# Optimization experiments

Hardware: AMD Instinct MI355X
Metric: run time of the kernel (lower is better)

The kernel has to match this reference:

```python
import jax, jax.numpy as jnp
import numpy as np

B, T, D, V = 64, 512, 1024, 28


def setup_inputs() -> dict:
    key = jax.random.key(0)
    ks = jax.random.split(key, 8)
    s = 0.05  # 'random_normal' keras initializer stddev
    return {
        "x": jax.random.normal(ks[0], (B, T, D), jnp.float32),
        "Wa": jax.random.normal(ks[1], (V, 1), jnp.float32) * s,
        "Ua": jax.random.normal(ks[2], (D, 1), jnp.float32) * s,
        "Va": jax.random.normal(ks[3], (1, 1), jnp.float32) * s,
        "Wo": jax.random.normal(ks[4], (V, 1), jnp.float32) * s,
        "Uo": jax.random.normal(ks[5], (D, V), jnp.float32) * s,
        "Co": jax.random.normal(ks[6], (D, V), jnp.float32) * s,
        "emb_table": jax.random.normal(ks[7], (V, V), jnp.float32) * s,
    }


def reference(x, Wa, Ua, Va, Wo, Uo, Co, emb_table):
    # x: [B, T, D]
    Bs, Ts, Ds = x.shape
    UaH = x @ Ua                                   # [B,T,1], step-invariant
    # Hanterior at step t is x[:, t-1] (zeros at t=0): it is updated AFTER y_t
    h_prev_seq = jnp.concatenate(
        [jnp.zeros((Bs, 1, Ds), x.dtype), x[:, :-1]], axis=1)  # [B,T,D]

    def step(y_prev, h_prev):
        # y_prev: [B,V]   h_prev: [B,D]
        WaS = y_prev @ Wa                          # [B,1]
        scores = jnp.tanh(UaH + WaS[:, None, :]) @ Va   # [B,T,1]
        # original applies softmax over the last (size-1) axis -> all ones; kept faithful
        scores = jax.nn.softmax(scores, axis=-1)
        c = jnp.einsum('btd,bt->bd', x, scores[..., 0])  # [B,D] context
        # keras Embedding casts its (float) input to int indices
        idx = y_prev.astype(jnp.int32)             # [B,V], values in [0, V)
        emb_res = emb_table[idx]                   # [B,V,V]
        WoE = (emb_res @ Wo)[..., 0]               # [B,V]
        y = jax.nn.sigmoid(WoE + h_prev @ Uo + c @ Co)   # [B,V]
        return y, y

    y0 = jnp.zeros((Bs, V), x.dtype)
    _, ys = jax.lax.scan(step, y0, jnp.swapaxes(h_prev_seq, 0, 1))  # [T,B,V]
    return jnp.swapaxes(ys, 0, 1)                  # [B,T,V]
```

## Files before the change

### kernel.cpp

```cpp
#include <hip/hip_runtime.h>
#include <cstddef>

#define BB 64
#define TT 512
#define DD 1024
#define VV 28
#define BV (BB * VV)

__global__ __launch_bounds__(256, 4) void k1_hU_rowsum(
    const float* __restrict__ x, const float* __restrict__ Uo,
    float* __restrict__ hU, float* __restrict__ part) {
  __shared__ float xs[32][68];
  __shared__ float Wl[64][32];
  const int g   = blockIdx.x;
  const int b   = g >> 4;
  const int tch = g & 15;
  const int t0  = tch << 5;
  const int tid = threadIdx.x;
  const int row = tid & 31;
  const int vg  = tid >> 5;
  const int vbase = vg << 2;
  float acc[4] = {0.f, 0.f, 0.f, 0.f};
  const float* xbase = x + (size_t)(b * TT + t0) * DD;

  for (int c = 0; c < 16; ++c) {
    const int d0 = c << 6;
    __syncthreads();
#pragma unroll
    for (int i = 0; i < 2; ++i) {
      const int f = tid + (i << 8);
      const int r = f >> 4;
      const int col = (f & 15) << 2;
      *reinterpret_cast<float4*>(&xs[r][col]) =
          *reinterpret_cast<const float4*>(xbase + (size_t)r * DD + d0 + col);
    }
#pragma unroll
    for (int k = 0; k < 8; ++k) {
      const int idx = tid + (k << 8);
      const int r = idx >> 5, ccol = idx & 31;
      Wl[r][ccol] = (ccol < VV) ? Uo[(size_t)(d0 + r) * VV + ccol] : 0.f;
    }
    __syncthreads();
#pragma unroll 2
    for (int dd = 0; dd < 64; dd += 4) {
      const float4 xv = *reinterpret_cast<const float4*>(&xs[row][dd]);
      const float xq[4] = {xv.x, xv.y, xv.z, xv.w};
#pragma unroll
      for (int q = 0; q < 4; ++q) {
        const float4 wa = *reinterpret_cast<const float4*>(&Wl[dd + q][vbase]);
        acc[0] = fmaf(xq[q], wa.x, acc[0]);
        acc[1] = fmaf(xq[q], wa.y, acc[1]);
        acc[2] = fmaf(xq[q], wa.z, acc[2]);
        acc[3] = fmaf(xq[q], wa.w, acc[3]);
      }
    }
    if (tid < 64) {
      float s = 0.f;
#pragma unroll 8
      for (int r = 0; r < 32; ++r) s += xs[r][tid];
      part[(size_t)(b * 16 + tch) * DD + d0 + tid] = s;
    }
  }
  const int t = t0 + row;
  if (t + 1 < TT && vbase < VV) {
    float* o = hU + (size_t)(t + 1) * BV + b * VV + vbase;
    *reinterpret_cast<float4*>(o) = make_float4(acc[0], acc[1], acc[2], acc[3]);
  }
}

__global__ __launch_bounds__(256) void k2_ctx_ew(
    const float* __restrict__ part, const float* __restrict__ Co,
    const float* __restrict__ Wo, const float* __restrict__ emb,
    float* __restrict__ ctx, float* __restrict__ ew) {
  __shared__ float rs[DD];
  __shared__ float red[8][32];
  const int b = blockIdx.x;
  const int tid = threadIdx.x;
  for (int d = tid; d < DD; d += 256) {
    float s = 0.f;
#pragma unroll
    for (int k = 0; k < 16; ++k) s += part[(size_t)(b * 16 + k) * DD + d];
    rs[d] = s;
  }
  __syncthreads();
  const int v = tid & 31, seg = tid >> 5;
  float pa = 0.f;
  if (v < VV) {
    const float* cp = Co + (size_t)(seg * 128) * VV + v;
    const float* rp = &rs[seg * 128];
#pragma unroll 4
    for (int d = 0; d < 128; ++d) pa = fmaf(rp[d], cp[(size_t)d * VV], pa);
  }
  red[seg][v] = pa;
  __syncthreads();
  if (tid < 32) {
    float s = 0.f;
#pragma unroll
    for (int k = 0; k < 8; ++k) s += red[k][tid];
    if (tid < VV) ctx[b * VV + tid] = s;
  }
  if (b == 0 && tid >= 64 && tid < 64 + VV) {
    const int j = tid - 64;
    float s = 0.f;
#pragma unroll
    for (int k = 0; k < VV; ++k) s = fmaf(emb[j * VV + k], Wo[k], s);
    ew[j] = s;
  }
}

__global__ __launch_bounds__(256) void k3a_bits(
    const float* __restrict__ hU, const float* __restrict__ ctx,
    const float* __restrict__ ew,
    unsigned long long* __restrict__ W0, unsigned long long* __restrict__ W1) {
  const int flat = blockIdx.x * 256 + threadIdx.x;
  const int t = flat / BV;
  const int bv = flat - t * BV;
  const float ctxv = ctx[bv];
  const float e0 = ew[0] + ctxv;
  const float e1 = ew[1] + ctxv;
  const float h = (t == 0) ? 0.f : hU[(size_t)t * BV + bv];
  const float c0 = 1.f / (1.f + expf(-(e0 + h)));
  const float c1 = 1.f / (1.f + expf(-(e1 + h)));
  const unsigned long long m0 = __ballot(c0 == 1.0f);
  const unsigned long long m1 = __ballot(c1 == 1.0f);
  if ((threadIdx.x & 63) == 0) {
    const int w = bv >> 6;
    W0[t * 28 + w] = m0;
    W1[t * 28 + w] = m1;
  }
}

__global__ __launch_bounds__(64) void k3b_scan(
    const unsigned long long* __restrict__ W0,
    const unsigned long long* __restrict__ W1,
    unsigned long long* __restrict__ S) {
  __shared__ unsigned long long l0[TT], l1[TT], ls[TT];
  const int j = blockIdx.x;
  const int tid = threadIdx.x;
  for (int t = tid; t < TT; t += 64) {
    l0[t] = W0[t * 28 + j];
    l1[t] = W1[t * 28 + j];
  }
  __syncthreads();
  if (tid == 0) {
    unsigned long long s = 0ull;
#pragma unroll 8
    for (int t = 0; t < TT; ++t) {
      ls[t] = s;
      s = (s & l1[t]) | (~s & l0[t]);
    }
  }
  __syncthreads();
  for (int t = tid; t < TT; t += 64) S[t * 28 + j] = ls[t];
}

__global__ __launch_bounds__(256) void k3c_out(
    const float* __restrict__ hU, const float* __restrict__ ctx,
    const float* __restrict__ ew, const unsigned long long* __restrict__ S,
    float* __restrict__ out) {
  const int flat = blockIdx.x * 256 + threadIdx.x;
  const int t = flat / BV;
  const int bv = flat - t * BV;
  const int b = bv / VV;
  const int v = bv - b * VV;
  const float ctxv = ctx[bv];
  const float h = (t == 0) ? 0.f : hU[(size_t)t * BV + bv];
  const unsigned long long w = S[t * 28 + (bv >> 6)];
  const float e = ((w >> (bv & 63)) & 1ull) ? ew[1] : ew[0];
  const float y = 1.f / (1.f + expf(-((e + ctxv) + h)));
  out[(size_t)b * TT * VV + (size_t)t * VV + v] = y;
}

extern "C" void kernel_launch(void* const* d_in, const int* in_sizes, int n_in,
                              void* d_out, int out_size, void* d_ws, size_t ws_size,
                              hipStream_t stream) {
  const float* x   = (const float*)d_in[0];
  const float* Wo  = (const float*)d_in[4];
  const float* Uo  = (const float*)d_in[5];
  const float* Co  = (const float*)d_in[6];
  const float* emb = (const float*)d_in[7];
  float* out = (float*)d_out;

  float* ws   = (float*)d_ws;
  float* hU   = ws;
  float* part = hU + (size_t)TT * BV;
  float* ctx  = part + (size_t)BB * 16 * DD;
  float* ewp  = ctx + BV;
  unsigned long long* W0 = (unsigned long long*)(ewp + 32);
  unsigned long long* W1 = W0 + (size_t)TT * 28;
  unsigned long long* S  = W1 + (size_t)TT * 28;

  k1_hU_rowsum<<<1024, 256, 0, stream>>>(x, Uo, hU, part);
  k2_ctx_ew<<<BB, 256, 0, stream>>>(part, Co, Wo, emb, ctx, ewp);
  k3a_bits<<<3584, 256, 0, stream>>>(hU, ctx, ewp, W0, W1);
  k3b_scan<<<28, 64, 0, stream>>>(W0, W1, S);
  k3c_out<<<3584, 256, 0, stream>>>(hU, ctx, ewp, S, out);
}
```

Baseline: 307.5 us.

## Restructure x@Uo kernel: one row per thread, all 28 outputs, split-D partials

```diff
diff --git a/kernel.cpp b/kernel.cpp
--- a/kernel.cpp
+++ b/kernel.cpp
@@ -7,64 +7,72 @@
 #define VV 28
 #define BV (BB * VV)
 
-__global__ __launch_bounds__(256, 4) void k1_hU_rowsum(
+template <int NDS>
+__global__ __launch_bounds__(256, 2) void k1_hU_rowsum(
     const float* __restrict__ x, const float* __restrict__ Uo,
-    float* __restrict__ hU, float* __restrict__ part) {
-  __shared__ float xs[32][68];
-  __shared__ float Wl[64][32];
+    float* __restrict__ hUp, float* __restrict__ part) {
+  constexpr int DPB = DD / NDS;
+  constexpr int NCH = DPB / 64;
+  __shared__ float xs[256][68];
   const int g   = blockIdx.x;
-  const int b   = g >> 4;
-  const int tch = g & 15;
-  const int t0  = tch << 5;
+  const int ds  = g % NDS;
+  const int r0  = g / NDS;
+  const int tch = r0 & 1;
+  const int b   = r0 >> 1;
+  const int t0  = tch << 8;
   const int tid = threadIdx.x;
-  const int row = tid & 31;
-  const int vg  = tid >> 5;
-  const int vbase = vg << 2;
-  float acc[4] = {0.f, 0.f, 0.f, 0.f};
-  const float* xbase = x + (size_t)(b * TT + t0) * DD;
-
-  for (int c = 0; c < 16; ++c) {
+  const int dbase = ds * DPB;
+  const float* xbase = x + (size_t)(b * TT + t0) * DD + dbase;
+  float acc[VV];
+#pragma unroll
+  for (int v = 0; v < VV; ++v) acc[v] = 0.f;
+  const int rcol = tid & 63;
+  const int rq   = tid >> 6;
+
+  for (int c = 0; c < NCH; ++c) {
     const int d0 = c << 6;
     __syncthreads();
 #pragma unroll
-    for (int i = 0; i < 2; ++i) {
-      const int f = tid + (i << 8);
-      const int r = f >> 4;
-      const int col = (f & 15) << 2;
-      *reinterpret_cast<float4*>(&xs[r][col]) =
-          *reinterpret_cast<const float4*>(xbase + (size_t)r * DD + d0 + col);
-    }
-#pragma unroll
-    for (int k = 0; k < 8; ++k) {
-      const int idx = tid + (k << 8);
-      const int r = idx >> 5, ccol = idx & 31;
-      Wl[r][ccol] = (ccol < VV) ? Uo[(size_t)(d0 + r) * VV + ccol] : 0.f;
+    for (int i = 0; i < 16; ++i) {
+      const int f   = tid + (i << 8);
+      const int row = f >> 4;
+      const int q4  = (f & 15) << 2;
+      *reinterpret_cast<float4*>(&xs[row][q4]) =
+          *reinterpret_cast<const float4*>(xbase + (size_t)row * DD + d0 + q4);
     }
     __syncthreads();
+    const float* uo = Uo + (size_t)(dbase + d0) * VV;
 #pragma unroll 2
     for (int dd = 0; dd < 64; dd += 4) {
-      const float4 xv = *reinterpret_cast<const float4*>(&xs[row][dd]);
+      const float4 xv = *reinterpret_cast<const float4*>(&xs[tid][dd]);
       const float xq[4] = {xv.x, xv.y, xv.z, xv.w};
 #pragma unroll
       for (int q = 0; q < 4; ++q) {
-        const float4 wa = *reinterpret_cast<const float4*>(&Wl[dd + q][vbase]);
-        acc[0] = fmaf(xq[q], wa.x, acc[0]);
-        acc[1] = fmaf(xq[q], wa.y, acc[1]);
-        acc[2] = fmaf(xq[q], wa.z, acc[2]);
-        acc[3] = fmaf(xq[q], wa.w, acc[3]);
+        const float* ur = uo + (size_t)(dd + q) * VV;
+#pragma unroll
+        for (int v7 = 0; v7 < 7; ++v7) {
+          const float4 w = *reinterpret_cast<const float4*>(ur + (v7 << 2));
+          acc[v7 * 4 + 0] = fmaf(xq[q], w.x, acc[v7 * 4 + 0]);
+          acc[v7 * 4 + 1] = fmaf(xq[q], w.y, acc[v7 * 4 + 1]);
+          acc[v7 * 4 + 2] = fmaf(xq[q], w.z, acc[v7 * 4 + 2]);
+          acc[v7 * 4 + 3] = fmaf(xq[q], w.w, acc[v7 * 4 + 3]);
+        }
       }
     }
-    if (tid < 64) {
+    {
       float s = 0.f;
 #pragma unroll 8
-      for (int r = 0; r < 32; ++r) s += xs[r][tid];
-      part[(size_t)(b * 16 + tch) * DD + d0 + tid] = s;
-    }
-  }
-  const int t = t0 + row;
-  if (t + 1 < TT && vbase < VV) {
-    float* o = hU + (size_t)(t + 1) * BV + b * VV + vbase;
-    *reinterpret_cast<float4*>(o) = make_float4(acc[0], acc[1], acc[2], acc[3]);
+      for (int r = 0; r < 64; ++r) s += xs[(rq << 6) + r][rcol];
+      part[(size_t)(b * 8 + tch * 4 + rq) * DD + dbase + d0 + rcol] = s;
+    }
+  }
+  const int t = t0 + tid;
+  if (t + 1 < TT) {
+    float* o = hUp + (size_t)ds * TT * BV + (size_t)(t + 1) * BV + b * VV;
+#pragma unroll
+    for (int v7 = 0; v7 < 7; ++v7)
+      *reinterpret_cast<float4*>(o + (v7 << 2)) = make_float4(
+          acc[v7 * 4 + 0], acc[v7 * 4 + 1], acc[v7 * 4 + 2], acc[v7 * 4 + 3]);
   }
 }
 
@@ -79,7 +87,7 @@
   for (int d = tid; d < DD; d += 256) {
     float s = 0.f;
 #pragma unroll
-    for (int k = 0; k < 16; ++k) s += part[(size_t)(b * 16 + k) * DD + d];
+    for (int k = 0; k < 8; ++k) s += part[(size_t)(b * 8 + k) * DD + d];
     rs[d] = s;
   }
   __syncthreads();
@@ -108,17 +116,23 @@
   }
 }
 
+template <int NDS>
 __global__ __launch_bounds__(256) void k3a_bits(
-    const float* __restrict__ hU, const float* __restrict__ ctx,
+    const float* __restrict__ hUp, const float* __restrict__ ctx,
     const float* __restrict__ ew,
     unsigned long long* __restrict__ W0, unsigned long long* __restrict__ W1) {
+  constexpr size_t PL = (size_t)TT * BV;
   const int flat = blockIdx.x * 256 + threadIdx.x;
   const int t = flat / BV;
   const int bv = flat - t * BV;
   const float ctxv = ctx[bv];
   const float e0 = ew[0] + ctxv;
   const float e1 = ew[1] + ctxv;
-  const float h = (t == 0) ? 0.f : hU[(size_t)t * BV + bv];
+  float h = 0.f;
+  if (t > 0) {
+#pragma unroll
+    for (int p = 0; p < NDS; ++p) h += hUp[(size_t)p * PL + (size_t)t * BV + bv];
+  }
   const float c0 = 1.f / (1.f + expf(-(e0 + h)));
   const float c1 = 1.f / (1.f + expf(-(e1 + h)));
   const unsigned long long m0 = __ballot(c0 == 1.0f);
@@ -154,17 +168,23 @@
   for (int t = tid; t < TT; t += 64) S[t * 28 + j] = ls[t];
 }
 
+template <int NDS>
 __global__ __launch_bounds__(256) void k3c_out(
-    const float* __restrict__ hU, const float* __restrict__ ctx,
+    const float* __restrict__ hUp, const float* __restrict__ ctx,
     const float* __restrict__ ew, const unsigned long long* __restrict__ S,
     float* __restrict__ out) {
+  constexpr size_t PL = (size_t)TT * BV;
   const int flat = blockIdx.x * 256 + threadIdx.x;
   const int t = flat / BV;
   const int bv = flat - t * BV;
   const int b = bv / VV;
   const int v = bv - b * VV;
   const float ctxv = ctx[bv];
-  const float h = (t == 0) ? 0.f : hU[(size_t)t * BV + bv];
+  float h = 0.f;
+  if (t > 0) {
+#pragma unroll
+    for (int p = 0; p < NDS; ++p) h += hUp[(size_t)p * PL + (size_t)t * BV + bv];
+  }
   const unsigned long long w = S[t * 28 + (bv >> 6)];
   const float e = ((w >> (bv & 63)) & 1ull) ? ew[1] : ew[0];
   const float y = 1.f / (1.f + expf(-((e + ctxv) + h)));
@@ -181,18 +201,37 @@
   const float* emb = (const float*)d_in[7];
   float* out = (float*)d_out;
 
-  float* ws   = (float*)d_ws;
-  float* hU   = ws;
-  float* part = hU + (size_t)TT * BV;
-  float* ctx  = part + (size_t)BB * 16 * DD;
-  float* ewp  = ctx + BV;
-  unsigned long long* W0 = (unsigned long long*)(ewp + 32);
-  unsigned long long* W1 = W0 + (size_t)TT * 28;
-  unsigned long long* S  = W1 + (size_t)TT * 28;
-
-  k1_hU_rowsum<<<1024, 256, 0, stream>>>(x, Uo, hU, part);
-  k2_ctx_ew<<<BB, 256, 0, stream>>>(part, Co, Wo, emb, ctx, ewp);
-  k3a_bits<<<3584, 256, 0, stream>>>(hU, ctx, ewp, W0, W1);
-  k3b_scan<<<28, 64, 0, stream>>>(W0, W1, S);
-  k3c_out<<<3584, 256, 0, stream>>>(hU, ctx, ewp, S, out);
-}
+  const size_t PL   = (size_t)TT * BV;
+  const size_t PART = (size_t)BB * 8 * DD;
+  const size_t need4 =
+      (4 * PL + PART + BV + 32) * sizeof(float) + 3 * (size_t)TT * 28 * 8;
+
+  float* ws = (float*)d_ws;
+  if (ws_size >= need4) {
+    float* hUp  = ws;
+    float* part = hUp + 4 * PL;
+    float* ctx  = part + PART;
+    float* ewp  = ctx + BV;
+    unsigned long long* W0 = (unsigned long long*)(ewp + 32);
+    unsigned long long* W1 = W0 + (size_t)TT * 28;
+    unsigned long long* S  = W1 + (size_t)TT * 28;
+    k1_hU_rowsum<4><<<64 * 2 * 4, 256, 0, stream>>>(x, Uo, hUp, part);
+    k2_ctx_ew<<<BB, 256, 0, stream>>>(part, Co, Wo, emb, ctx, ewp);
+    k3a_bits<4><<<3584, 256, 0, stream>>>(hUp, ctx, ewp, W0, W1);
+    k3b_scan<<<28, 64, 0, stream>>>(W0, W1, S);
+    k3c_out<4><<<3584, 256, 0, stream>>>(hUp, ctx, ewp, S, out);
+  } else {
+    float* hUp  = ws;
+    float* part = hUp + PL;
+    float* ctx  = part + PART;
+    float* ewp  = ctx + BV;
+    unsigned long long* W0 = (unsigned long long*)(ewp + 32);
+    unsigned long long* W1 = W0 + (size_t)TT * 28;
+    unsigned long long* S  = W1 + (size_t)TT * 28;
+    k1_hU_rowsum<1><<<64 * 2, 256, 0, stream>>>(x, Uo, hUp, part);
+    k2_ctx_ew<<<BB, 256, 0, stream>>>(part, Co, Wo, emb, ctx, ewp);
+    k3a_bits<1><<<3584, 256, 0, stream>>>(hUp, ctx, ewp, W0, W1);
+    k3b_scan<<<28, 64, 0, stream>>>(W0, W1, S);
+    k3c_out<1><<<3584, 256, 0, stream>>>(hUp, ctx, ewp, S, out);
+  }
+}
```

Result: no change. 305.5 us (-0.6%).

## Compute hidden projection with bf16 MFMA and double-buffered shared-memory pipeline

Applied to the files above, without the earlier changes.

```diff
diff --git a/kernel.cpp b/kernel.cpp
--- a/kernel.cpp
+++ b/kernel.cpp
@@ -7,65 +7,133 @@
 #define VV 28
 #define BV (BB * VV)
 
-__global__ __launch_bounds__(256, 4) void k1_hU_rowsum(
-    const float* __restrict__ x, const float* __restrict__ Uo,
+typedef float f32x4 __attribute__((ext_vector_type(4)));
+typedef short bf16x8 __attribute__((ext_vector_type(8)));
+
+static __device__ __forceinline__ ushort f2bf(float f) {
+  unsigned u = __float_as_uint(f);
+  unsigned r = (u + 0x7FFF + ((u >> 16) & 1)) >> 16;
+  return (ushort)r;
+}
+
+__global__ __launch_bounds__(256) void k0_packB(const float* __restrict__ Uo,
+                                                ushort* __restrict__ Ubf) {
+  const int idx = blockIdx.x * 256 + threadIdx.x;
+  const int v = idx >> 10, k = idx & 1023;
+  const float f = (v < VV) ? Uo[(size_t)k * VV + v] : 0.f;
+  Ubf[idx] = f2bf(f);
+}
+
+__global__ __launch_bounds__(256, 2) void k1_mfma(
+    const float* __restrict__ x, const ushort* __restrict__ Ubf,
     float* __restrict__ hU, float* __restrict__ part) {
-  __shared__ float xs[32][68];
-  __shared__ float Wl[64][32];
-  const int g   = blockIdx.x;
-  const int b   = g >> 4;
-  const int tch = g & 15;
-  const int t0  = tch << 5;
+  __shared__ ushort Ab[2][64 * 128];
+  __shared__ ushort Bb[2][32 * 128];
+  __shared__ float rsum[8][128];
+  const int g = blockIdx.x, b = g >> 3, tch = g & 7;
   const int tid = threadIdx.x;
-  const int row = tid & 31;
-  const int vg  = tid >> 5;
-  const int vbase = vg << 2;
-  float acc[4] = {0.f, 0.f, 0.f, 0.f};
-  const float* xbase = x + (size_t)(b * TT + t0) * DD;
-
-  for (int c = 0; c < 16; ++c) {
-    const int d0 = c << 6;
-    __syncthreads();
-#pragma unroll
-    for (int i = 0; i < 2; ++i) {
-      const int f = tid + (i << 8);
-      const int r = f >> 4;
-      const int col = (f & 15) << 2;
-      *reinterpret_cast<float4*>(&xs[r][col]) =
-          *reinterpret_cast<const float4*>(xbase + (size_t)r * DD + d0 + col);
+  const int w = tid >> 6, l = tid & 63;
+  const float* xbase = x + (size_t)(b * TT + tch * 64) * DD;
+  const int srow0 = tid >> 5;
+  const int scol4 = (tid & 31) << 2;
+  const int bv_ = tid >> 3;
+  const int bseg = (tid & 7) << 4;
+  const int arow = 16 * w + (l & 15);
+  const int aswz = (arow & 7) << 4;
+  const int bcol0 = l & 15, bcol1 = 16 + (l & 15);
+  const int bswz0 = (bcol0 & 7) << 4, bswz1 = (bcol1 & 7) << 4;
+  const int kg16 = (l >> 4) << 4;
+
+  f32x4 acc0 = {0.f, 0.f, 0.f, 0.f}, acc1 = {0.f, 0.f, 0.f, 0.f};
+  float4 ld[8];
+  uint4 bl0, bl1;
+
+#define ISSUE(c)                                                              \
+  {                                                                           \
+    const float* p = xbase + (c) * 128;                                       \
+    _Pragma("unroll") for (int i = 0; i < 8; ++i) {                           \
+      ld[i] = *reinterpret_cast<const float4*>(                               \
+          p + (size_t)(srow0 + 8 * i) * DD + scol4);                          \
+    }                                                                         \
+    const ushort* q = Ubf + bv_ * 1024 + (c) * 128 + bseg;                    \
+    bl0 = *reinterpret_cast<const uint4*>(q);                                 \
+    bl1 = *reinterpret_cast<const uint4*>(q + 8);                             \
+  }
+
+#define WRITE(buf)                                                            \
+  {                                                                           \
+    float4 ps = make_float4(0.f, 0.f, 0.f, 0.f);                              \
+    _Pragma("unroll") for (int i = 0; i < 8; ++i) {                           \
+      ps.x += ld[i].x; ps.y += ld[i].y; ps.z += ld[i].z; ps.w += ld[i].w;     \
+      const int row = srow0 + 8 * i;                                          \
+      ushort4 hv;                                                             \
+      hv.x = f2bf(ld[i].x); hv.y = f2bf(ld[i].y);                             \
+      hv.z = f2bf(ld[i].z); hv.w = f2bf(ld[i].w);                             \
+      *reinterpret_cast<ushort4*>(                                            \
+          (char*)&Ab[buf][0] + ((row * 256 + scol4 * 2) ^ ((row & 7) << 4))) = \
+          hv;                                                                 \
+    }                                                                         \
+    *reinterpret_cast<uint4*>(                                                \
+        (char*)&Bb[buf][0] + ((bv_ * 256 + bseg * 2) ^ ((bv_ & 7) << 4))) =   \
+        bl0;                                                                  \
+    *reinterpret_cast<uint4*>(                                                \
+        (char*)&Bb[buf][0] +                                                  \
+        ((bv_ * 256 + bseg * 2 + 16) ^ ((bv_ & 7) << 4))) = bl1;              \
+    *reinterpret_cast<float4*>(&rsum[srow0][scol4]) = ps;                     \
+  }
+
+#define REDUCE(c)                                                             \
+  if (tid < 128) {                                                            \
+    float s_ = 0.f;                                                           \
+    _Pragma("unroll") for (int g2 = 0; g2 < 8; ++g2) s_ += rsum[g2][tid];     \
+    part[(size_t)(b * 8 + tch) * DD + (c) * 128 + tid] = s_;                  \
+  }
+
+#define COMPUTE(cb)                                                           \
+  {                                                                           \
+    _Pragma("unroll") for (int s = 0; s < 4; ++s) {                           \
+      const int kb = s * 64 + kg16;                                           \
+      bf16x8 af = *reinterpret_cast<const bf16x8*>(                           \
+          (const char*)&Ab[cb][0] + ((arow * 256 + kb) ^ aswz));              \
+      bf16x8 b0f = *reinterpret_cast<const bf16x8*>(                          \
+          (const char*)&Bb[cb][0] + ((bcol0 * 256 + kb) ^ bswz0));            \
+      bf16x8 b1f = *reinterpret_cast<const bf16x8*>(                          \
+          (const char*)&Bb[cb][0] + ((bcol1 * 256 + kb) ^ bswz1));            \
+      acc0 = __builtin_amdgcn_mfma_f32_16x16x32_bf16(af, b0f, acc0, 0, 0, 0); \
+      acc1 = __builtin_amdgcn_mfma_f32_16x16x32_bf16(af, b1f, acc1, 0, 0, 0); \
+    }                                                                         \
+  }
+
+  ISSUE(0);
+  WRITE(0);
+  __syncthreads();
+  REDUCE(0);
+  for (int c = 0; c < 8; ++c) {
+    if (c < 7) ISSUE(c + 1);
+    COMPUTE(c & 1);
+    if (c < 7) {
+      __syncthreads();
+      WRITE((c + 1) & 1);
+      __syncthreads();
+      REDUCE(c + 1);
     }
-#pragma unroll
-    for (int k = 0; k < 8; ++k) {
-      const int idx = tid + (k << 8);
-      const int r = idx >> 5, ccol = idx & 31;
-      Wl[r][ccol] = (ccol < VV) ? Uo[(size_t)(d0 + r) * VV + ccol] : 0.f;
+  }
+
+  const int tb = tch * 64 + 16 * w + ((l >> 4) << 2);
+  const int v0 = l & 15;
+#pragma unroll
+  for (int r = 0; r < 4; ++r) {
+    const int t = tb + r;
+    if (t + 1 < TT) {
+      float* o = hU + (size_t)(t + 1) * BV + b * VV;
+      o[v0] = acc0[r];
+      if (v0 + 16 < VV) o[v0 + 16] = acc1[r];
     }
-    __syncthreads();
-#pragma unroll 2
-    for (int dd = 0; dd < 64; dd += 4) {
-      const float4 xv = *reinterpret_cast<const float4*>(&xs[row][dd]);
-      const float xq[4] = {xv.x, xv.y, xv.z, xv.w};
-#pragma unroll
-      for (int q = 0; q < 4; ++q) {
-        const float4 wa = *reinterpret_cast<const float4*>(&Wl[dd + q][vbase]);
-        acc[0] = fmaf(xq[q], wa.x, acc[0]);
-        acc[1] = fmaf(xq[q], wa.y, acc[1]);
-        acc[2] = fmaf(xq[q], wa.z, acc[2]);
-        acc[3] = fmaf(xq[q], wa.w, acc[3]);
-      }
-    }
-    if (tid < 64) {
-      float s = 0.f;
-#pragma unroll 8
-      for (int r = 0; r < 32; ++r) s += xs[r][tid];
-      part[(size_t)(b * 16 + tch) * DD + d0 + tid] = s;
-    }
-  }
-  const int t = t0 + row;
-  if (t + 1 < TT && vbase < VV) {
-    float* o = hU + (size_t)(t + 1) * BV + b * VV + vbase;
-    *reinterpret_cast<float4*>(o) = make_float4(acc[0], acc[1], acc[2], acc[3]);
-  }
+  }
+#undef ISSUE
+#undef WRITE
+#undef REDUCE
+#undef COMPUTE
 }
 
 __global__ __launch_bounds__(256) void k2_ctx_ew(
@@ -79,7 +147,7 @@
   for (int d = tid; d < DD; d += 256) {
     float s = 0.f;
 #pragma unroll
-    for (int k = 0; k < 16; ++k) s += part[(size_t)(b * 16 + k) * DD + d];
+    for (int k = 0; k < 8; ++k) s += part[(size_t)(b * 8 + k) * DD + d];
     rs[d] = s;
   }
   __syncthreads();
@@ -124,9 +192,9 @@
   const unsigned long long m0 = __ballot(c0 == 1.0f);
   const unsigned long long m1 = __ballot(c1 == 1.0f);
   if ((threadIdx.x & 63) == 0) {
-    const int w = bv >> 6;
-    W0[t * 28 + w] = m0;
-    W1[t * 28 + w] = m1;
+    const int wq = bv >> 6;
+    W0[t * 28 + wq] = m0;
+    W1[t * 28 + wq] = m1;
   }
 }
 
@@ -165,8 +233,8 @@
   const int v = bv - b * VV;
   const float ctxv = ctx[bv];
   const float h = (t == 0) ? 0.f : hU[(size_t)t * BV + bv];
-  const unsigned long long w = S[t * 28 + (bv >> 6)];
-  const float e = ((w >> (bv & 63)) & 1ull) ? ew[1] : ew[0];
+  const unsigned long long wq = S[t * 28 + (bv >> 6)];
+  const float e = ((wq >> (bv & 63)) & 1ull) ? ew[1] : ew[0];
   const float y = 1.f / (1.f + expf(-((e + ctxv) + h)));
   out[(size_t)b * TT * VV + (size_t)t * VV + v] = y;
 }
@@ -184,13 +252,15 @@
   float* ws   = (float*)d_ws;
   float* hU   = ws;
   float* part = hU + (size_t)TT * BV;
-  float* ctx  = part + (size_t)BB * 16 * DD;
+  float* ctx  = part + (size_t)BB * 8 * DD;
   float* ewp  = ctx + BV;
   unsigned long long* W0 = (unsigned long long*)(ewp + 32);
   unsigned long long* W1 = W0 + (size_t)TT * 28;
   unsigned long long* S  = W1 + (size_t)TT * 28;
-
-  k1_hU_rowsum<<<1024, 256, 0, stream>>>(x, Uo, hU, part);
+  ushort* Ubf = (ushort*)(S + (size_t)TT * 28);
+
+  k0_packB<<<128, 256, 0, stream>>>(Uo, Ubf);
+  k1_mfma<<<512, 256, 0, stream>>>(x, Ubf, hU, part);
   k2_ctx_ew<<<BB, 256, 0, stream>>>(part, Co, Wo, emb, ctx, ewp);
   k3a_bits<<<3584, 256, 0, stream>>>(hU, ctx, ewp, W0, W1);
   k3b_scan<<<28, 64, 0, stream>>>(W0, W1, S);
```

Result: faster. 254.3 us (-17.3%).
